# Optimization experiments

Measured on AMD Instinct MI355X. Metric: run time of the kernel, lower is better.

Reference implementation:

```python
import jax, jax.numpy as jnp
import numpy as np

NUM_E_BITS = 5
NUM_M_BITS = 10
EXP_BIAS = 2 ** (NUM_E_BITS - 1) - 1  # 15


def float2bit(f):
    """Faithful vectorized port of torch float2bit (num_e_bits=5, num_m_bits=10).

    Only the first NUM_M_BITS mantissa bits are computed (the torch code computes
    127 and slices [..., :num_m_bits]; the sliced-away bits never affect output).
    """
    dt = f.dtype
    is_nan = jnp.isnan(f)
    is_inf = jnp.isinf(f)
    is_neg_inf = is_inf & (f < 0)
    is_pos_inf = is_inf & (f > 0)
    is_normal = ~(is_nan | is_inf)

    fsafe = jnp.where(is_normal, f, jnp.asarray(1.0, dt))  # avoid nan/inf math
    # sign bit: (sign(v + 0.001) * -1 + 1) * 0.5
    s = (jnp.sign(fsafe + 0.001) * -1.0 + 1.0) * 0.5
    f1 = jnp.abs(fsafe)
    e_sci = jnp.floor(jnp.log2(f1))
    # log2(0) -> -inf gets clamped to -(2^(E-1)-1)
    e_sci = jnp.where(jnp.isneginf(e_sci), jnp.asarray(-float(EXP_BIAS), dt), e_sci)
    e_dec = e_sci + EXP_BIAS

    # integer2bit: bits k = floor(e_dec / 2^k) % 2 for k = E-1 .. 0
    e_pows = (2.0 ** jnp.arange(NUM_E_BITS - 1, -1, -1)).astype(dt)  # [16,8,4,2,1]
    e_bits = jnp.mod(jnp.floor(e_dec[..., None] / e_pows), 2.0)

    f2 = f1 / (2.0 ** e_sci)
    r = jnp.mod(f2, 1.0)
    m_pows = (2.0 ** jnp.arange(NUM_M_BITS)).astype(dt)
    m_bits = jnp.floor(2.0 * jnp.mod(r[..., None] * m_pows, 1.0))

    bits = jnp.concatenate([s[..., None], e_bits, m_bits], axis=-1)  # [..., 16]

    # special-value patterns
    z1 = jnp.zeros((1,), dt)
    o1 = jnp.ones((1,), dt)
    oe = jnp.ones((NUM_E_BITS,), dt)
    zm = jnp.zeros((NUM_M_BITS,), dt)
    nan_pat = jnp.concatenate([z1, oe, o1, jnp.zeros((NUM_M_BITS - 1,), dt)])
    pinf_pat = jnp.concatenate([z1, oe, zm])
    ninf_pat = jnp.concatenate([o1, oe, zm])
    bits = jnp.where(is_nan[..., None], nan_pat, bits)
    bits = jnp.where(is_pos_inf[..., None], pinf_pat, bits)
    bits = jnp.where(is_neg_inf[..., None], ninf_pat, bits)
    return bits


def setup_inputs() -> dict:
    key = jax.random.key(0)
    x = jax.random.normal(key, (256, 2048, 4), dtype=jnp.float32)
    return {"x": x}


def reference(x):
    bits = float2bit(x)  # [B, S, input_size, 16]
    out = bits.reshape(*bits.shape[:-2], bits.shape[-2] * bits.shape[-1])
    return (out - 0.5) * 2.0
```

## Files before the change

kernel.cpp:

```cpp
#include <hip/hip_runtime.h>
#include <hip/hip_fp16.h>


typedef float vfloat4 __attribute__((ext_vector_type(4)));

__device__ __forceinline__ unsigned decode_w(float f) {
  unsigned u = __float_as_uint(f);
  unsigned a = u & 0x7FFFFFFFu;
  unsigned w;
  if (__builtin_expect(a - 0x38800000u < 0x0F000000u, 1)) {
    float tm = __uint_as_float(a & 0xFFFFE000u);
    w = (unsigned)__half_as_ushort(__float2half(tm));
  } else if (a > 0x7F800000u) {
    w = 0x7E00u;
  } else if (a == 0x7F800000u) {
    w = 0x7C00u;
  } else if (a == 0u) {
    w = 0u;
  } else {
    int e8 = (int)(a >> 23);
    int E; unsigned mant;
    if (e8 != 0) {
      E = e8 - 127;
      mant = a & 0x7FFFFFu;
    } else {
      int p = 31 - __clz((int)a);
      E = p - 149;
      mant = (a << (23 - p)) & 0x7FFFFFu;
    }
    w = ((unsigned)((E + 15) & 31) << 10) | (mant >> 13);
  }
  float tt = f + 0.001f;
  if (tt < 0.0f) w |= 0x8000u;
  return w;
}

__device__ __forceinline__ vfloat4 extract4(unsigned w, int sh, bool szero) {
  unsigned nib = w >> sh;
  vfloat4 o;
  o.x = __uint_as_float(0xBF800000u ^ ((nib << 28) & 0x80000000u));
  o.y = __uint_as_float(0xBF800000u ^ ((nib << 29) & 0x80000000u));
  o.z = __uint_as_float(0xBF800000u ^ ((nib << 30) & 0x80000000u));
  o.w = __uint_as_float(0xBF800000u ^ (nib << 31));
  if (szero) o.x = 0.0f;
  return o;
}

__global__ __launch_bounds__(256) void preencoder_f2b_kernel(
    const float* __restrict__ x, vfloat4* __restrict__ out, int n4) {
  const int S = gridDim.x * blockDim.x;
  const int tid = blockIdx.x * blockDim.x + threadIdx.x;
  const int c = tid & 3;
  const int sh = 12 - 4 * c;

  if (n4 == 16 * S) {
    const int S4 = S >> 2;
    int t = tid;
    int e = tid >> 2;
    float f[4];
#pragma unroll
    for (int j = 0; j < 4; ++j) f[j] = x[e + j * S4];

#pragma unroll
    for (int r = 0; r < 4; ++r) {
      float g[4] = {0.0f, 0.0f, 0.0f, 0.0f};
      if (r < 3) {
        int en = e + S;
#pragma unroll
        for (int j = 0; j < 4; ++j) g[j] = x[en + j * S4];
      }
#pragma unroll
      for (int j = 0; j < 4; ++j) {
        bool szero = (c == 0) && (f[j] == -0.001f);
        out[t + j * S] = extract4(decode_w(f[j]), sh, szero);
      }
#pragma unroll
      for (int j = 0; j < 4; ++j) f[j] = g[j];
      e += S;
      t += 4 * S;
    }
  } else {
    for (int t = tid; t < n4; t += S) {
      int cc = t & 3;
      bool szero = (cc == 0) && (x[t >> 2] == -0.001f);
      out[t] = extract4(decode_w(x[t >> 2]), 12 - 4 * cc, szero);
    }
  }
}

extern "C" void kernel_launch(void* const* d_in, const int* in_sizes, int n_in,
                              void* d_out, int out_size, void* d_ws, size_t ws_size,
                              hipStream_t stream) {
  const float* x = (const float*)d_in[0];
  vfloat4* out = (vfloat4*)d_out;
  int n4 = out_size / 4;
  int threads = 256;
  int blocks = 2048;
  preencoder_f2b_kernel<<<blocks, threads, 0, stream>>>(x, out, n4);
}
```

Baseline: 141.1 us.

## Split encoding into pack kernel and expand kernel via workspace buffer

Replaces the single fused kernel with two kernels. The first decodes each input float into a packed 16-bit pattern plus a flag and writes it to a workspace buffer. The second expands those packed words into the ±1 float output. The aim is to keep the per-element decode off the store-heavy expansion path. The cost is an extra launch and an extra global write and read of the packed buffer, and the workspace must be large enough to hold it.

```diff
diff --git a/kernel.cpp b/kernel.cpp
--- a/kernel.cpp
+++ b/kernel.cpp
@@ -3,6 +3,7 @@
 
 
 typedef float vfloat4 __attribute__((ext_vector_type(4)));
+typedef float vfloat4h __attribute__((ext_vector_type(4)));
 
 __device__ __forceinline__ unsigned decode_w(float f) {
   unsigned u = __float_as_uint(f);
@@ -30,61 +31,63 @@
     }
     w = ((unsigned)((E + 15) & 31) << 10) | (mant >> 13);
   }
-  float tt = f + 0.001f;
-  if (tt < 0.0f) w |= 0x8000u;
+  if (f + 0.001f < 0.0f) w |= 0x8000u;
   return w;
 }
 
-__device__ __forceinline__ vfloat4 extract4(unsigned w, int sh, bool szero) {
-  unsigned nib = w >> sh;
-  vfloat4 o;
-  o.x = __uint_as_float(0xBF800000u ^ ((nib << 28) & 0x80000000u));
-  o.y = __uint_as_float(0xBF800000u ^ ((nib << 29) & 0x80000000u));
-  o.z = __uint_as_float(0xBF800000u ^ ((nib << 30) & 0x80000000u));
-  o.w = __uint_as_float(0xBF800000u ^ (nib << 31));
-  if (szero) o.x = 0.0f;
-  return o;
+__global__ __launch_bounds__(256) void pack_kernel(
+    const float* __restrict__ x, unsigned* __restrict__ packed, int n) {
+  const int S = gridDim.x * blockDim.x;
+  const int tid = blockIdx.x * blockDim.x + threadIdx.x;
+  int nv = n >> 2;
+  const vfloat4* x4 = (const vfloat4*)x;
+  for (int i = tid; i < nv; i += S) {
+    vfloat4 f = x4[i];
+    unsigned p0 = decode_w(f.x) | ((f.x == -0.001f) ? 0x10000u : 0u);
+    unsigned p1 = decode_w(f.y) | ((f.y == -0.001f) ? 0x10000u : 0u);
+    unsigned p2 = decode_w(f.z) | ((f.z == -0.001f) ? 0x10000u : 0u);
+    unsigned p3 = decode_w(f.w) | ((f.w == -0.001f) ? 0x10000u : 0u);
+    uint4 o; o.x = p0; o.y = p1; o.z = p2; o.w = p3;
+    ((uint4*)packed)[i] = o;
+  }
+  for (int i = (nv << 2) + tid; i < n; i += S) {
+    float f = x[i];
+    packed[i] = decode_w(f) | ((f == -0.001f) ? 0x10000u : 0u);
+  }
 }
 
-__global__ __launch_bounds__(256) void preencoder_f2b_kernel(
-    const float* __restrict__ x, vfloat4* __restrict__ out, int n4) {
+__global__ __launch_bounds__(256) void expand_kernel(
+    const unsigned* __restrict__ packed, vfloat4* __restrict__ out, int n4) {
   const int S = gridDim.x * blockDim.x;
-  const int tid = blockIdx.x * blockDim.x + threadIdx.x;
-  const int c = tid & 3;
-  const int sh = 12 - 4 * c;
+  int t = blockIdx.x * blockDim.x + threadIdx.x;
 
-  if (n4 == 16 * S) {
-    const int S4 = S >> 2;
-    int t = tid;
-    int e = tid >> 2;
-    float f[4];
+  for (; t + 3 * S < n4; t += 4 * S) {
 #pragma unroll
-    for (int j = 0; j < 4; ++j) f[j] = x[e + j * S4];
-
-#pragma unroll
-    for (int r = 0; r < 4; ++r) {
-      float g[4] = {0.0f, 0.0f, 0.0f, 0.0f};
-      if (r < 3) {
-        int en = e + S;
-#pragma unroll
-        for (int j = 0; j < 4; ++j) g[j] = x[en + j * S4];
-      }
-#pragma unroll
-      for (int j = 0; j < 4; ++j) {
-        bool szero = (c == 0) && (f[j] == -0.001f);
-        out[t + j * S] = extract4(decode_w(f[j]), sh, szero);
-      }
-#pragma unroll
-      for (int j = 0; j < 4; ++j) f[j] = g[j];
-      e += S;
-      t += 4 * S;
+    for (int j = 0; j < 4; ++j) {
+      int tj = t + j * S;
+      unsigned v = packed[tj >> 2];
+      int c = tj & 3;
+      unsigned nib = v >> (12 - 4 * c);
+      vfloat4 o;
+      o.x = __uint_as_float(0xBF800000u ^ ((nib << 28) & 0x80000000u));
+      o.y = __uint_as_float(0xBF800000u ^ ((nib << 29) & 0x80000000u));
+      o.z = __uint_as_float(0xBF800000u ^ ((nib << 30) & 0x80000000u));
+      o.w = __uint_as_float(0xBF800000u ^ (nib << 31));
+      if (c == 0 && (v & 0x10000u)) o.x = 0.0f;
+      out[tj] = o;
     }
-  } else {
-    for (int t = tid; t < n4; t += S) {
-      int cc = t & 3;
-      bool szero = (cc == 0) && (x[t >> 2] == -0.001f);
-      out[t] = extract4(decode_w(x[t >> 2]), 12 - 4 * cc, szero);
-    }
+  }
+  for (; t < n4; t += S) {
+    unsigned v = packed[t >> 2];
+    int c = t & 3;
+    unsigned nib = v >> (12 - 4 * c);
+    vfloat4 o;
+    o.x = __uint_as_float(0xBF800000u ^ ((nib << 28) & 0x80000000u));
+    o.y = __uint_as_float(0xBF800000u ^ ((nib << 29) & 0x80000000u));
+    o.z = __uint_as_float(0xBF800000u ^ ((nib << 30) & 0x80000000u));
+    o.w = __uint_as_float(0xBF800000u ^ (nib << 31));
+    if (c == 0 && (v & 0x10000u)) o.x = 0.0f;
+    out[t] = o;
   }
 }
 
@@ -93,8 +96,11 @@
                               hipStream_t stream) {
   const float* x = (const float*)d_in[0];
   vfloat4* out = (vfloat4*)d_out;
+  unsigned* packed = (unsigned*)d_ws;
+  int n = in_sizes[0];
   int n4 = out_size / 4;
   int threads = 256;
   int blocks = 2048;
-  preencoder_f2b_kernel<<<blocks, threads, 0, stream>>>(x, out, n4);
+  pack_kernel<<<1024, threads, 0, stream>>>(x, packed, n);
+  expand_kernel<<<blocks, threads, 0, stream>>>(packed, out, n4);
 }
```

Result: no change. 141.8 us (+0.5%).
